# Kernel optimization log

Measured on AMD Instinct MI355X. Metric: run time of the kernel, lower is better.

## Reference

```python
import math
import jax, jax.numpy as jnp
import numpy as np

N_HEADS = 8
WINDOW = 4


def _get_relative_embeddings(emb, length, window):
    # emb: [1, 2*window+1, k_channels] -> [1, 2*length-1, k_channels]
    pad_length = max(length - (window + 1), 0)
    start = max(window + 1 - length, 0)
    if pad_length > 0:
        emb = jnp.pad(emb, ((0, 0), (pad_length, pad_length), (0, 0)))
    return emb[:, start:start + 2 * length - 1]


def _relative_position_to_absolute_position(x):
    # x: [b, h, l, 2l-1] -> [b, h, l, l] (skewing trick)
    b, h, l, _ = x.shape
    x = jnp.pad(x, ((0, 0), (0, 0), (0, 0), (0, 1)))
    x_flat = x.reshape(b, h, l * 2 * l)
    x_flat = jnp.pad(x_flat, ((0, 0), (0, 0), (0, l - 1)))
    return x_flat.reshape(b, h, l + 1, 2 * l - 1)[:, :, :l, l - 1:]


def _absolute_position_to_relative_position(x):
    # x: [b, h, l, l] -> [b, h, l, 2l-1]
    b, h, l, _ = x.shape
    x = jnp.pad(x, ((0, 0), (0, 0), (0, 0), (0, l - 1)))
    x_flat = x.reshape(b, h, l * l + l * (l - 1))
    x_flat = jnp.pad(x_flat, ((0, 0), (0, 0), (l, 0)))
    return x_flat.reshape(b, h, l, 2 * l)[:, :, :, 1:]


def setup_inputs() -> dict:
    key = jax.random.key(0)
    ks = jax.random.split(key, 12)
    b, t, d = 4, 1024, 512
    kc = d // N_HEADS
    s = 1.0 / math.sqrt(d)
    return {
        "x": jax.random.normal(ks[0], (b, t, d), jnp.float32),
        "c": jax.random.normal(ks[1], (b, t, d), jnp.float32),
        "wq": jax.random.normal(ks[2], (d, d), jnp.float32) * s,
        "bq": jnp.zeros((d,), jnp.float32),
        "wk": jax.random.normal(ks[3], (d, d), jnp.float32) * s,
        "bk": jnp.zeros((d,), jnp.float32),
        "wv": jax.random.normal(ks[4], (d, d), jnp.float32) * s,
        "bv": jnp.zeros((d,), jnp.float32),
        "wo": jax.random.normal(ks[5], (d, d), jnp.float32) * s,
        "bo": jnp.zeros((d,), jnp.float32),
        "emb_rel_k": jax.random.normal(ks[6], (1, 2 * WINDOW + 1, kc), jnp.float32) * kc ** -0.5,
        "emb_rel_v": jax.random.normal(ks[7], (1, 2 * WINDOW + 1, kc), jnp.float32) * kc ** -0.5,
    }


def reference(x, c, wq, bq, wk, bk, wv, bv, wo, bo, emb_rel_k, emb_rel_v):
    b, t, d = x.shape
    h = N_HEADS
    kc = d // h
    inv_sqrt = 1.0 / math.sqrt(kc)

    # 1x1 conv projections (pointwise matmul)
    q = x @ wq + bq   # [b, t, d]
    k = c @ wk + bk
    v = c @ wv + bv

    # Faithful reshape as in source: [b, t, d] -> [b, h, kc, t] -> [b, h, t, kc]
    q = q.reshape(b, h, kc, t).transpose(0, 1, 3, 2)
    k = k.reshape(b, h, kc, t).transpose(0, 1, 3, 2)
    v = v.reshape(b, h, kc, t).transpose(0, 1, 3, 2)

    scores = jnp.einsum('bhtd,bhsd->bhts', q, k) * inv_sqrt  # [b,h,t,t]

    # relative key logits
    key_rel = _get_relative_embeddings(emb_rel_k, t, WINDOW)[0]  # [2t-1, kc]
    rel_logits = jnp.einsum('bhtd,md->bhtm', q, key_rel)          # [b,h,t,2t-1]
    scores_local = _relative_position_to_absolute_position(rel_logits) * inv_sqrt
    scores = scores + scores_local

    p_attn = jax.nn.softmax(scores, axis=-1)
    output = jnp.einsum('bhts,bhsd->bhtd', p_attn, v)  # [b,h,t,kc]

    # relative value contribution
    rel_weights = _absolute_position_to_relative_position(p_attn)  # [b,h,t,2t-1]
    val_rel = _get_relative_embeddings(emb_rel_v, t, WINDOW)[0]    # [2t-1, kc]
    output = output + jnp.einsum('bhtm,md->bhtd', rel_weights, val_rel)

    # Faithful output reshape: [b,h,t,kc] -> [b,h,kc,t] -> [b,t,d]
    output = output.transpose(0, 1, 3, 2).reshape(b, t, d)
    out = output @ wo + bo
    return out
```

## Files before the change

### kernel.cpp

```cpp
#include <hip/hip_runtime.h>
#include <hip/hip_bf16.h>

#define NB 4
#define NT 1024
#define ND 512
#define NH 8
#define NKC 64

typedef __bf16 bf16x8 __attribute__((ext_vector_type(8)));
typedef float f32x4 __attribute__((ext_vector_type(4)));
typedef unsigned int u32;

__device__ __forceinline__ f32x4 MFMA(bf16x8 a, bf16x8 b, f32x4 c) {
    return __builtin_amdgcn_mfma_f32_16x16x32_bf16(a, b, c, 0, 0, 0);
}
__device__ __forceinline__ unsigned short f2bu(float v) {
    __hip_bfloat16 b = __float2bfloat16(v);
    return *(unsigned short*)&b;
}
__device__ __forceinline__ void split1(float v, unsigned short& h, unsigned short& l)
{
    __hip_bfloat16 hb = __float2bfloat16(v);
    float r = v - __bfloat162float(hb);
    __hip_bfloat16 lb = __float2bfloat16(r);
    h = *(unsigned short*)&hb;
    l = *(unsigned short*)&lb;
}
__device__ __forceinline__ void splitpack(const float4 a, const float4 b, uint4& h, uint4& l)
{
    union { unsigned short u[8]; uint4 v; } H, L;
    const float f[8] = {a.x, a.y, a.z, a.w, b.x, b.y, b.z, b.w};
    #pragma unroll
    for (int j = 0; j < 8; ++j) split1(f[j], H.u[j], L.u[j]);
    h = H.v; l = L.v;
}
__device__ __forceinline__ void gl16(const unsigned short* g, unsigned short* l) {
    __builtin_amdgcn_global_load_lds(
        (const __attribute__((address_space(1))) u32*)g,
        (__attribute__((address_space(3))) u32*)l, 16, 0, 0);
}

__global__ __launch_bounds__(256)
void splitT_kernel(const float* __restrict__ w0, const float* __restrict__ w1,
                   const float* __restrict__ w2, const float* __restrict__ w3,
                   unsigned short* __restrict__ wT)
{
    __shared__ float tl[32][33];
    const float* w = (blockIdx.z == 0) ? w0 : (blockIdx.z == 1) ? w1
                   : (blockIdx.z == 2) ? w2 : w3;
    unsigned short* hi = wT + (size_t)blockIdx.z * 2 * (ND * ND);
    unsigned short* lo = hi + ND * ND;
    const int t = threadIdx.x;
    const int x0 = blockIdx.x * 32, y0 = blockIdx.y * 32;
    {
        const int r = t >> 3, c = (t & 7) * 4;
        const float4 v = *(const float4*)&w[(size_t)(y0 + r) * ND + x0 + c];
        tl[r][c] = v.x; tl[r][c+1] = v.y; tl[r][c+2] = v.z; tl[r][c+3] = v.w;
    }
    __syncthreads();
    {
        const int nr = t >> 3, k4 = (t & 7) * 4;
        unsigned short hh[4], ll[4];
        #pragma unroll
        for (int j = 0; j < 4; ++j) split1(tl[k4 + j][nr], hh[j], ll[j]);
        ushort4 h = make_ushort4(hh[0], hh[1], hh[2], hh[3]);
        ushort4 l = make_ushort4(ll[0], ll[1], ll[2], ll[3]);
        *(ushort4*)&hi[(size_t)(x0 + nr) * ND + y0 + k4] = h;
        *(ushort4*)&lo[(size_t)(x0 + nr) * ND + y0 + k4] = l;
    }
}

__global__ __launch_bounds__(256, 3)
void proj_mfma(const float* __restrict__ x, const float* __restrict__ cc,
               const unsigned short* __restrict__ wT,
               const float* __restrict__ bq, const float* __restrict__ bk,
               const float* __restrict__ bv,
               unsigned short* __restrict__ qh_o, unsigned short* __restrict__ ql_o,
               unsigned short* __restrict__ kh_o, unsigned short* __restrict__ vh_o)
{
    __shared__ unsigned short smem[13312];
    unsigned short* Ah = smem;
    unsigned short* Al = smem + 2560;
    unsigned short* Bh = smem + 5120;
    unsigned short* Bl = smem + 9216;
    unsigned short* Tr = smem;

    const int hw = blockIdx.x + 4 * blockIdx.y + 256 * blockIdx.z;
    const int swz = (hw & 7) * 96 + (hw >> 3);
    const int xt = swz & 3;
    const int yt = (swz >> 2) & 63;
    const int which = swz >> 8;

    const float* A_g = (which == 0) ? x : cc;
    const unsigned short* Bh_g = wT + (size_t)which * 2 * (ND * ND);
    const unsigned short* Bl_g = Bh_g + ND * ND;
    const float* bias = (which == 0) ? bq : (which == 1) ? bk : bv;

    const int tid = threadIdx.x, l = tid & 63, w = tid >> 6;
    const int quad = l >> 4, lc = l & 15;
    const int wm = w & 1, wn = w >> 1;
    const int n0 = xt * 128, m0 = yt * 64;

    const int am = tid >> 2, ak = (tid & 3) * 8;
    const size_t aG = (size_t)(m0 + am) * ND + ak;

    const int lr = l >> 2, lc4 = l & 3;
    const int lcs = lc4 ^ ((lr >> 1) & 3);
    const unsigned short* bsrcH0 = Bh_g + (size_t)(n0 + w * 32 + lr) * ND + lcs * 8;
    const unsigned short* bsrcH1 = bsrcH0 + 16 * ND;
    const unsigned short* bsrcL0 = Bl_g + (size_t)(n0 + w * 32 + lr) * ND + lcs * 8;
    const unsigned short* bsrcL1 = bsrcL0 + 16 * ND;
    unsigned short* bdstH0 = Bh + (w * 32) * 32;
    unsigned short* bdstH1 = Bh + (w * 32 + 16) * 32;
    unsigned short* bdstL0 = Bl + (w * 32) * 32;
    unsigned short* bdstL1 = Bl + (w * 32 + 16) * 32;

    float4 ra0 = *(const float4*)&A_g[aG];
    float4 ra1 = *(const float4*)&A_g[aG + 4];
    uint4 h0, l0;
    splitpack(ra0, ra1, h0, l0);

    const int fsw = (lc >> 1) & 3;
    const int bchunk = (quad ^ fsw) * 8;

    f32x4 acc[2][4];
    #pragma unroll
    for (int mi = 0; mi < 2; ++mi)
        #pragma unroll
        for (int ni = 0; ni < 4; ++ni) acc[mi][ni] = (f32x4){0.f, 0.f, 0.f, 0.f};

    for (int k0 = 0; k0 < ND; k0 += 32) {
        __syncthreads();
        {
            *(uint4*)&Ah[am * 40 + ak] = h0;
            *(uint4*)&Al[am * 40 + ak] = l0;
            gl16(bsrcH0 + k0, bdstH0);
            gl16(bsrcH1 + k0, bdstH1);
            gl16(bsrcL0 + k0, bdstL0);
            gl16(bsrcL1 + k0, bdstL1);
        }
        __syncthreads();
        if (k0 + 32 < ND) {
            const size_t aN = aG + k0 + 32;
            ra0 = *(const float4*)&A_g[aN];
            ra1 = *(const float4*)&A_g[aN + 4];
        }

        bf16x8 ah[2], al2[2], bh[4], bl[4];
        #pragma unroll
        for (int mi = 0; mi < 2; ++mi) {
            const int ar = (wm * 32 + mi * 16 + lc) * 40 + quad * 8;
            ah[mi] = *(const bf16x8*)&Ah[ar];
            al2[mi] = *(const bf16x8*)&Al[ar];
        }
        #pragma unroll
        for (int ni = 0; ni < 4; ++ni) {
            const int br = (wn * 64 + ni * 16 + lc) * 32 + bchunk;
            bh[ni] = *(const bf16x8*)&Bh[br];
            bl[ni] = *(const bf16x8*)&Bl[br];
        }
        #pragma unroll
        for (int mi = 0; mi < 2; ++mi)
            #pragma unroll
            for (int ni = 0; ni < 4; ++ni) {
                acc[mi][ni] = MFMA(al2[mi], bh[ni], acc[mi][ni]);
                acc[mi][ni] = MFMA(ah[mi], bl[ni], acc[mi][ni]);
                acc[mi][ni] = MFMA(ah[mi], bh[ni], acc[mi][ni]);
            }
        if (k0 + 32 < ND) splitpack(ra0, ra1, h0, l0);
    }

    const int bb = m0 >> 10, tt0 = m0 & 1023;
    const int hh = tt0 >> 7, cch0 = (tt0 & 127) >> 1;
    const int bh_idx = bb * NH + hh;

    if (which == 2) {
        #pragma unroll
        for (int ni = 0; ni < 4; ++ni) {
            const int n = n0 + wn * 64 + ni * 16 + lc;
            const float bval = bias[n];
            #pragma unroll
            for (int mi = 0; mi < 2; ++mi)
                #pragma unroll
                for (int r = 0; r < 4; ++r) {
                    const int mloc = wm * 32 + mi * 16 + quad * 4 + r;
                    const int cch = cch0 + (mloc >> 1);
                    const int t = (mloc & 1) * 512 + n;
                    vh_o[(((size_t)bh_idx * 16 + (t >> 6)) * 64 + cch) * 64 + (t & 63)] =
                        f2bu(acc[mi][ni][r] + bval);
                }
        }
        return;
    }

    const int npass = (which == 0) ? 2 : 1;
    unsigned short* outp[2] = {(which == 0) ? qh_o : kh_o, ql_o};

    for (int pass = 0; pass < npass; ++pass) {
        __syncthreads();
        #pragma unroll
        for (int ni = 0; ni < 4; ++ni) {
            const int nloc = wn * 64 + ni * 16 + lc;
            const float bval = bias[n0 + nloc];
            #pragma unroll
            for (int mi = 0; mi < 2; ++mi)
                #pragma unroll
                for (int r = 0; r < 4; ++r) {
                    const int mloc = wm * 32 + mi * 16 + quad * 4 + r;
                    const float val = acc[mi][ni][r] + bval;
                    unsigned short hs, ls;
                    if (which == 0) { split1(val, hs, ls); }
                    else { hs = f2bu(val); ls = 0; }
                    Tr[((mloc & 1) * 128 + nloc) * 40 + (mloc >> 1)] =
                        (pass == 0) ? hs : ls;
                }
        }
        __syncthreads();
        {
            const int t = (tid >> 7) * 512 + n0 + (tid & 127);
            const size_t oa = ((size_t)bh_idx * NT + t) * NKC + cch0;
            const uint4 v0 = *(const uint4*)&Tr[tid * 40];
            const uint4 v1 = *(const uint4*)&Tr[tid * 40 + 8];
            const uint4 v2 = *(const uint4*)&Tr[tid * 40 + 16];
            const uint4 v3 = *(const uint4*)&Tr[tid * 40 + 24];
            *(uint4*)&outp[pass][oa]      = v0;
            *(uint4*)&outp[pass][oa + 8]  = v1;
            *(uint4*)&outp[pass][oa + 16] = v2;
            *(uint4*)&outp[pass][oa + 24] = v3;
        }
    }
}

__global__ __launch_bounds__(256, 4)
void outproj_mfma(const unsigned short* __restrict__ a_g,
                  const unsigned short* __restrict__ wTh,
                  const float* __restrict__ bo, float* __restrict__ out)
{
    __shared__ unsigned short smem2[6144];
    unsigned short* As = smem2;
    unsigned short* Bh = smem2 + 2048;
    unsigned short* Bl = smem2 + 4096;
    const unsigned short* Bl_g = wTh + ND * ND;
    const int tid = threadIdx.x, l = tid & 63, w = tid >> 6;
    const int quad = l >> 4, lc = l & 15;
    const int wm = w & 1, wn = w >> 1;

    const int hw = blockIdx.x + 8 * blockIdx.y;
    const int swz = (hw & 7) * 64 + (hw >> 3);
    const int n0 = (swz & 7) * 64, m0 = (swz >> 3) * 64;

    const int lr = l >> 2, lc4 = l & 3;
    const int lcs = lc4 ^ ((lr >> 1) & 3);
    const unsigned short* asrc  = a_g + (size_t)(m0 + w * 16 + lr) * ND + lcs * 8;
    const unsigned short* bhsrc = wTh + (size_t)(n0 + w * 16 + lr) * ND + lcs * 8;
    const unsigned short* blsrc = Bl_g + (size_t)(n0 + w * 16 + lr) * ND + lcs * 8;
    unsigned short* adst = As + (w * 16) * 32;
    unsigned short* bhdst = Bh + (w * 16) * 32;
    unsigned short* bldst = Bl + (w * 16) * 32;

    const int fsw = (lc >> 1) & 3;
    const int chunk = (quad ^ fsw) * 8;

    f32x4 acc[2][2];
    #pragma unroll
    for (int mi = 0; mi < 2; ++mi)
        #pragma unroll
        for (int ni = 0; ni < 2; ++ni) acc[mi][ni] = (f32x4){0.f, 0.f, 0.f, 0.f};

    for (int k0 = 0; k0 < ND; k0 += 32) {
        __syncthreads();
        gl16(asrc + k0, adst);
        gl16(bhsrc + k0, bhdst);
        gl16(blsrc + k0, bldst);
        __syncthreads();

        bf16x8 ab[2], bhf[2], blf[2];
        #pragma unroll
        for (int mi = 0; mi < 2; ++mi)
            ab[mi] = *(const bf16x8*)&As[(wm * 32 + mi * 16 + lc) * 32 + chunk];
        #pragma unroll
        for (int ni = 0; ni < 2; ++ni) {
            const int br = (wn * 32 + ni * 16 + lc) * 32 + chunk;
            bhf[ni] = *(const bf16x8*)&Bh[br];
            blf[ni] = *(const bf16x8*)&Bl[br];
        }
        #pragma unroll
        for (int mi = 0; mi < 2; ++mi)
            #pragma unroll
            for (int ni = 0; ni < 2; ++ni) {
                acc[mi][ni] = MFMA(ab[mi], bhf[ni], acc[mi][ni]);
                acc[mi][ni] = MFMA(ab[mi], blf[ni], acc[mi][ni]);
            }
    }

    #pragma unroll
    for (int ni = 0; ni < 2; ++ni) {
        const int n = n0 + wn * 32 + ni * 16 + lc;
        const float bval = bo[n];
        #pragma unroll
        for (int mi = 0; mi < 2; ++mi)
            #pragma unroll
            for (int r = 0; r < 4; ++r) {
                const int m = m0 + wm * 32 + mi * 16 + quad * 4 + r;
                out[(size_t)m * ND + n] = acc[mi][ni][r] + bval;
            }
    }
}

__global__ __launch_bounds__(512, 4)
void attn_mfma(const unsigned short* __restrict__ qh_g, const unsigned short* __restrict__ ql_g,
               const unsigned short* __restrict__ kh_g,
               const unsigned short* __restrict__ vh_g,
               const float* __restrict__ embk, const float* __restrict__ embv,
               unsigned short* __restrict__ ath)
{
    __shared__ unsigned short smem[33792];
    unsigned short* Ev  = smem + 16384;
    unsigned short* Ps  = smem + 18944;
    float* bandv = (float*)(smem + 32256);
    unsigned short* EkH = smem + 18944;
    unsigned short* EkL = EkH + 1152;

    const int tid = threadIdx.x, l = tid & 63, w = tid >> 6;
    const int quad = l >> 4, lc = l & 15;
    const int g = w & 3;
    const int h = w >> 2;

    const int hw = blockIdx.x + 16 * blockIdx.y + 128 * blockIdx.z;
    const int swz = (hw & 7) * 64 + (hw >> 3);
    const int q0 = (swz & 15) * 64;
    const int hh = (swz >> 4) & 7, bb = swz >> 7;

    const int sBeg = h * 512;
    const int bh = bb * NH + hh;
    const size_t qkBase = (size_t)bh * NT * NKC;
    const size_t vtBase = (size_t)bh * (16 * 64 * 64);

    unsigned short* Ksh = smem + h * 4096;
    unsigned short* Vsh = smem + 8192 + h * 4096;

    const int tl = tid & 255;
    const int rr = tl >> 3, cc8 = tl & 7;
    const int cs = cc8 ^ (rr & 7);
    const unsigned short* kSrc = kh_g + qkBase + (size_t)(sBeg + rr) * NKC + cs * 8;
    const unsigned short* vSrc = vh_g + vtBase + (size_t)(sBeg >> 6) * 4096 + rr * 64 + cs * 8;
    const int wvh = tl >> 6;
    unsigned short* dK = Ksh + wvh * 512;
    unsigned short* dV = Vsh + wvh * 512;

    for (int idx = tid; idx < 16 * 72; idx += 512) {
        const int d = idx / 72, kc = idx - d * 72;
        const float v = (d < 9 && kc < 64) ? embk[d * 64 + kc] : 0.f;
        unsigned short hs, ls;
        split1(v, hs, ls);
        EkH[idx] = hs;
        EkL[idx] = ls;
    }
    for (int idx = tid; idx < 64 * 40; idx += 512) {
        const int c = idx / 40, d = idx - c * 40;
        Ev[idx] = f2bu((d < 9) ? embv[d * 64 + c] : 0.f);
    }
    __syncthreads();

    bf16x8 qh[2], ql[2];
    {
        const int qg = q0 + g * 16 + lc;
        const size_t qa = qkBase + (size_t)qg * NKC + quad * 8;
        qh[0] = *(const bf16x8*)&qh_g[qa];
        qh[1] = *(const bf16x8*)&qh_g[qa + 32];
        ql[0] = *(const bf16x8*)&ql_g[qa];
        ql[1] = *(const bf16x8*)&ql_g[qa + 32];
    }

    {
        f32x4 accB = (f32x4){0.f, 0.f, 0.f, 0.f};
        #pragma unroll
        for (int kk = 0; kk < 2; ++kk) {
            const bf16x8 ebh = *(const bf16x8*)&EkH[lc * 72 + kk * 32 + quad * 8];
            const bf16x8 ebl = *(const bf16x8*)&EkL[lc * 72 + kk * 32 + quad * 8];
            accB = MFMA(ql[kk], ebh, accB);
            accB = MFMA(qh[kk], ebl, accB);
            accB = MFMA(qh[kk], ebh, accB);
        }
        __syncthreads();
        if (h == 0 && lc <= 8) {
            #pragma unroll
            for (int r = 0; r < 4; ++r)
                bandv[(g * 16 + quad * 4 + r) * 12 + lc] = accB[r];
        }
    }
    unsigned short* P = Ps + w * 1664;
    {
        const int zr = l >> 2, zc = 64 + (l & 3) * 8;
        *(uint4*)&P[zr * 104 + zc] = (uint4){0u, 0u, 0u, 0u};
    }

    const int swz8 = lc & 7;

    f32x4 O[4];
    #pragma unroll
    for (int ci = 0; ci < 4; ++ci) O[ci] = (f32x4){0.f, 0.f, 0.f, 0.f};
    float l_run[4] = {0.f, 0.f, 0.f, 0.f};
    bool prevdiag = false;

    for (int s0 = sBeg; s0 < sBeg + 512; s0 += 64) {
        __syncthreads();
        gl16(kSrc, dK);  gl16(kSrc + 2048, dK + 2048);
        gl16(vSrc, dV);  gl16(vSrc + 2048, dV + 2048);
        kSrc += 4096; vSrc += 4096;
        __syncthreads();

        const int sd = s0 - q0;
        const bool diag = (sd >= -64) && (sd <= 64);

        f32x4 S[4];
        #pragma unroll
        for (int ni = 0; ni < 4; ++ni) {
            f32x4 a = (f32x4){0.f, 0.f, 0.f, 0.f};
            #pragma unroll
            for (int kk = 0; kk < 2; ++kk) {
                const bf16x8 kb = *(const bf16x8*)
                    &Ksh[(ni * 16 + lc) * 64 + ((kk * 4 + quad) ^ swz8) * 8];
                a = MFMA(ql[kk], kb, a);
                a = MFMA(qh[kk], kb, a);
            }
            S[ni] = a;
        }

        if (diag) {
            #pragma unroll
            for (int ni = 0; ni < 4; ++ni)
                #pragma unroll
                for (int r = 0; r < 4; ++r) {
                    const int ql64 = g * 16 + quad * 4 + r;
                    const int dp4 = (s0 + ni * 16 + lc) - (q0 + ql64) + 4;
                    if (dp4 >= 0 && dp4 <= 8) S[ni][r] += bandv[ql64 * 12 + dp4];
                }
        }
        #pragma unroll
        for (int ni = 0; ni < 4; ++ni)
            #pragma unroll
            for (int r = 0; r < 4; ++r)
                S[ni][r] = __expf(S[ni][r] * 0.125f);
        #pragma unroll
        for (int r = 0; r < 4; ++r)
            l_run[r] += S[0][r] + S[1][r] + S[2][r] + S[3][r];

        if (diag || prevdiag) {
            const int zr = l >> 2, zc = 64 + (l & 3) * 4;
            *(ushort4*)&P[zr * 104 + zc] = make_ushort4(0, 0, 0, 0);
        }
        if (diag) {
            #pragma unroll
            for (int ni = 0; ni < 4; ++ni)
                #pragma unroll
                for (int r = 0; r < 4; ++r) {
                    const int prow = quad * 4 + r;
                    const unsigned short pb = f2bu(S[ni][r]);
                    P[prow * 104 + ni * 16 + lc] = pb;
                    const int dp4 = (s0 + ni * 16 + lc) - (q0 + g * 16 + prow) + 4;
                    if (dp4 >= 0 && dp4 <= 8) P[prow * 104 + 64 + dp4] = pb;
                }
        } else {
            #pragma unroll
            for (int ni = 0; ni < 4; ++ni)
                #pragma unroll
                for (int r = 0; r < 4; ++r) {
                    const int prow = quad * 4 + r;
                    P[prow * 104 + ni * 16 + lc] = f2bu(S[ni][r]);
                }
        }

        #pragma unroll
        for (int ks = 0; ks < 2; ++ks) {
            const bf16x8 pa = *(const bf16x8*)&P[lc * 104 + ks * 32 + quad * 8];
            #pragma unroll
            for (int ci = 0; ci < 4; ++ci) {
                const bf16x8 vb = *(const bf16x8*)
                    &Vsh[(ci * 16 + lc) * 64 + ((ks * 4 + quad) ^ swz8) * 8];
                O[ci] = MFMA(pa, vb, O[ci]);
            }
        }
        {
            const bf16x8 pa = *(const bf16x8*)&P[lc * 104 + 64 + quad * 8];
            #pragma unroll
            for (int ci = 0; ci < 4; ++ci) {
                const bf16x8 vb = *(const bf16x8*)&Ev[(ci * 16 + lc) * 40 + quad * 8];
                O[ci] = MFMA(pa, vb, O[ci]);
            }
        }
        prevdiag = diag;
    }

    #pragma unroll
    for (int r = 0; r < 4; ++r) {
        float v = l_run[r];
        v += __shfl_xor(v, 1); v += __shfl_xor(v, 2);
        v += __shfl_xor(v, 4); v += __shfl_xor(v, 8);
        l_run[r] = v;
    }

    __syncthreads();
    float* Oex = (float*)smem;
    float* l1s = bandv;
    const int qloc0 = g * 16 + quad * 4;

    if (h == 1) {
        #pragma unroll
        for (int ci = 0; ci < 4; ++ci)
            #pragma unroll
            for (int r = 0; r < 4; ++r)
                Oex[(qloc0 + r) * 64 + ci * 16 + lc] = O[ci][r];
        if (lc == 0) {
            #pragma unroll
            for (int r = 0; r < 4; ++r)
                l1s[qloc0 + r] = l_run[r];
        }
    }
    __syncthreads();
    if (h == 0) {
        float linv[4];
        #pragma unroll
        for (int r = 0; r < 4; ++r)
            linv[r] = 1.f / (l_run[r] + l1s[qloc0 + r]);
        #pragma unroll
        for (int ci = 0; ci < 4; ++ci) {
            const int c = ci * 16 + lc;
            const int row = hh * 128 + 2 * c + (q0 >> 9);
            unsigned short o[4];
            #pragma unroll
            for (int r = 0; r < 4; ++r)
                o[r] = f2bu((O[ci][r] + Oex[(qloc0 + r) * 64 + c]) * linv[r]);
            *(ushort4*)&ath[((size_t)bb * NT + row) * ND + (q0 & 511) + qloc0] =
                make_ushort4(o[0], o[1], o[2], o[3]);
        }
    }
}

extern "C" void kernel_launch(void* const* d_in, const int* in_sizes, int n_in,
                              void* d_out, int out_size, void* d_ws, size_t ws_size,
                              hipStream_t stream) {
    const float* x    = (const float*)d_in[0];
    const float* c    = (const float*)d_in[1];
    const float* wq   = (const float*)d_in[2];
    const float* bq   = (const float*)d_in[3];
    const float* wk   = (const float*)d_in[4];
    const float* bk   = (const float*)d_in[5];
    const float* wv   = (const float*)d_in[6];
    const float* bv   = (const float*)d_in[7];
    const float* wo   = (const float*)d_in[8];
    const float* bo   = (const float*)d_in[9];
    const float* embk = (const float*)d_in[10];
    const float* embv = (const float*)d_in[11];

    unsigned short* u16 = (unsigned short*)d_ws;
    const size_t M = 1024 * 1024;
    unsigned short* wT  = u16;
    unsigned short* qh  = u16 + 2 * M;
    unsigned short* ql  = u16 + 4 * M;
    unsigned short* kh  = u16 + 6 * M;
    unsigned short* vh  = u16 + 8 * M;
    unsigned short* ath = u16 + 10 * M;

    splitT_kernel<<<dim3(16, 16, 4), 256, 0, stream>>>(wq, wk, wv, wo, wT);

    proj_mfma<<<dim3(4, 64, 3), 256, 0, stream>>>(x, c, wT, bq, bk, bv,
                                                  qh, ql, kh, vh);

    attn_mfma<<<dim3(16, 8, 4), 512, 0, stream>>>(qh, ql, kh, vh,
                                                  embk, embv, ath);

    outproj_mfma<<<dim3(8, 64), 256, 0, stream>>>(ath,
                                                  wT + (size_t)3 * 2 * ND * ND,
                                                  bo, (float*)d_out);
}
```

Before: 149.6 us.

## Load K/V MFMA fragments directly from global memory, dropping LDS staging

Replaces the shared-memory staging of K and V tiles, which needed two block-wide barriers per iteration, with per-lane direct global loads of the bf16x8 MFMA fragments. The shared-memory footprint roughly halves, which may allow more blocks per CU. The cost is that each group of waves sharing a head half now fetches the same K/V rows separately, multiplying global/L2 traffic. The loads may also be less coalesced and their latency is exposed without explicit staging.

```diff
diff --git a/kernel.cpp b/kernel.cpp
--- a/kernel.cpp
+++ b/kernel.cpp
@@ -314,11 +314,11 @@
                const float* __restrict__ embk, const float* __restrict__ embv,
                unsigned short* __restrict__ ath)
 {
-    __shared__ unsigned short smem[33792];
-    unsigned short* Ev  = smem + 16384;
-    unsigned short* Ps  = smem + 18944;
-    float* bandv = (float*)(smem + 32256);
-    unsigned short* EkH = smem + 18944;
+    __shared__ unsigned short smem[17408];
+    unsigned short* Ps  = smem;
+    unsigned short* Ev  = smem + 13312;
+    float* bandv = (float*)(smem + 15872);
+    unsigned short* EkH = smem;
     unsigned short* EkL = EkH + 1152;
 
     const int tid = threadIdx.x, l = tid & 63, w = tid >> 6;
@@ -335,18 +335,6 @@
     const int bh = bb * NH + hh;
     const size_t qkBase = (size_t)bh * NT * NKC;
     const size_t vtBase = (size_t)bh * (16 * 64 * 64);
-
-    unsigned short* Ksh = smem + h * 4096;
-    unsigned short* Vsh = smem + 8192 + h * 4096;
-
-    const int tl = tid & 255;
-    const int rr = tl >> 3, cc8 = tl & 7;
-    const int cs = cc8 ^ (rr & 7);
-    const unsigned short* kSrc = kh_g + qkBase + (size_t)(sBeg + rr) * NKC + cs * 8;
-    const unsigned short* vSrc = vh_g + vtBase + (size_t)(sBeg >> 6) * 4096 + rr * 64 + cs * 8;
-    const int wvh = tl >> 6;
-    unsigned short* dK = Ksh + wvh * 512;
-    unsigned short* dV = Vsh + wvh * 512;
 
     for (int idx = tid; idx < 16 * 72; idx += 512) {
         const int d = idx / 72, kc = idx - d * 72;
@@ -394,8 +382,10 @@
         const int zr = l >> 2, zc = 64 + (l & 3) * 8;
         *(uint4*)&P[zr * 104 + zc] = (uint4){0u, 0u, 0u, 0u};
     }
-
-    const int swz8 = lc & 7;
+    __syncthreads();
+
+    const unsigned short* kF = kh_g + qkBase + (size_t)(sBeg + lc) * NKC + quad * 8;
+    const unsigned short* vF = vh_g + vtBase + (size_t)(sBeg >> 6) * 4096 + lc * 64 + quad * 8;
 
     f32x4 O[4];
     #pragma unroll
@@ -404,28 +394,29 @@
     bool prevdiag = false;
 
     for (int s0 = sBeg; s0 < sBeg + 512; s0 += 64) {
-        __syncthreads();
-        gl16(kSrc, dK);  gl16(kSrc + 2048, dK + 2048);
-        gl16(vSrc, dV);  gl16(vSrc + 2048, dV + 2048);
-        kSrc += 4096; vSrc += 4096;
-        __syncthreads();
-
+        const int st = s0 - sBeg;
         const int sd = s0 - q0;
         const bool diag = (sd >= -64) && (sd <= 64);
 
         f32x4 S[4];
         #pragma unroll
         for (int ni = 0; ni < 4; ++ni) {
+            const bf16x8 k0 = *(const bf16x8*)&kF[(size_t)(st + ni * 16) * NKC];
+            const bf16x8 k1 = *(const bf16x8*)&kF[(size_t)(st + ni * 16) * NKC + 32];
             f32x4 a = (f32x4){0.f, 0.f, 0.f, 0.f};
-            #pragma unroll
-            for (int kk = 0; kk < 2; ++kk) {
-                const bf16x8 kb = *(const bf16x8*)
-                    &Ksh[(ni * 16 + lc) * 64 + ((kk * 4 + quad) ^ swz8) * 8];
-                a = MFMA(ql[kk], kb, a);
-                a = MFMA(qh[kk], kb, a);
-            }
+            a = MFMA(ql[0], k0, a);
+            a = MFMA(qh[0], k0, a);
+            a = MFMA(ql[1], k1, a);
+            a = MFMA(qh[1], k1, a);
             S[ni] = a;
         }
+
+        bf16x8 vf[4][2];
+        #pragma unroll
+        for (int ci = 0; ci < 4; ++ci)
+            #pragma unroll
+            for (int ks = 0; ks < 2; ++ks)
+                vf[ci][ks] = *(const bf16x8*)&vF[(size_t)(st >> 6) * 4096 + ci * 1024 + ks * 32];
 
         if (diag) {
             #pragma unroll
@@ -475,11 +466,8 @@
         for (int ks = 0; ks < 2; ++ks) {
             const bf16x8 pa = *(const bf16x8*)&P[lc * 104 + ks * 32 + quad * 8];
             #pragma unroll
-            for (int ci = 0; ci < 4; ++ci) {
-                const bf16x8 vb = *(const bf16x8*)
-                    &Vsh[(ci * 16 + lc) * 64 + ((ks * 4 + quad) ^ swz8) * 8];
-                O[ci] = MFMA(pa, vb, O[ci]);
-            }
+            for (int ci = 0; ci < 4; ++ci)
+                O[ci] = MFMA(pa, vf[ci][ks], O[ci]);
         }
         {
             const bf16x8 pa = *(const bf16x8*)&P[lc * 104 + 64 + quad * 8];
```

After: 184.4 us. 1.23x slower.

## Double-buffer LDS in projection GEMMs and skip relative-value MFMA off-diagonal

Applied to the files above, without the earlier changes.

The input and output projection GEMMs now use two LDS buffers. The next K-slice is staged while the current one is computed, which leaves one barrier per step instead of two and lets global loads overlap MFMA work. The attention kernel now runs the band relative-value MFMA, and zeroes its P columns, only on diagonal tiles rather than on every tile. Doubling shared memory may lower occupancy for the projection kernels, which request 3 and 4 blocks per CU.

```diff
diff --git a/kernel.cpp b/kernel.cpp
--- a/kernel.cpp
+++ b/kernel.cpp
@@ -78,11 +78,7 @@
                unsigned short* __restrict__ qh_o, unsigned short* __restrict__ ql_o,
                unsigned short* __restrict__ kh_o, unsigned short* __restrict__ vh_o)
 {
-    __shared__ unsigned short smem[13312];
-    unsigned short* Ah = smem;
-    unsigned short* Al = smem + 2560;
-    unsigned short* Bh = smem + 5120;
-    unsigned short* Bl = smem + 9216;
+    __shared__ unsigned short smem[26624];
     unsigned short* Tr = smem;
 
     const int hw = blockIdx.x + 4 * blockIdx.y + 256 * blockIdx.z;
@@ -110,64 +106,81 @@
     const unsigned short* bsrcH1 = bsrcH0 + 16 * ND;
     const unsigned short* bsrcL0 = Bl_g + (size_t)(n0 + w * 32 + lr) * ND + lcs * 8;
     const unsigned short* bsrcL1 = bsrcL0 + 16 * ND;
-    unsigned short* bdstH0 = Bh + (w * 32) * 32;
-    unsigned short* bdstH1 = Bh + (w * 32 + 16) * 32;
-    unsigned short* bdstL0 = Bl + (w * 32) * 32;
-    unsigned short* bdstL1 = Bl + (w * 32 + 16) * 32;
+
+    const int fsw = (lc >> 1) & 3;
+    const int bchunk = (quad ^ fsw) * 8;
+
+    f32x4 acc[2][4];
+    #pragma unroll
+    for (int mi = 0; mi < 2; ++mi)
+        #pragma unroll
+        for (int ni = 0; ni < 4; ++ni) acc[mi][ni] = (f32x4){0.f, 0.f, 0.f, 0.f};
+
+    auto STAGE = [&](unsigned short* base, int k0, const uint4& h, const uint4& lo4) {
+        *(uint4*)&base[am * 40 + ak] = h;
+        *(uint4*)&base[2560 + am * 40 + ak] = lo4;
+        gl16(bsrcH0 + k0, base + 5120 + w * 1024);
+        gl16(bsrcH1 + k0, base + 5120 + w * 1024 + 512);
+        gl16(bsrcL0 + k0, base + 9216 + w * 1024);
+        gl16(bsrcL1 + k0, base + 9216 + w * 1024 + 512);
+    };
+    auto COMPUTE = [&](const unsigned short* base) {
+        bf16x8 ah[2], al2[2], bhf[4], blf[4];
+        #pragma unroll
+        for (int mi = 0; mi < 2; ++mi) {
+            const int ar = (wm * 32 + mi * 16 + lc) * 40 + quad * 8;
+            ah[mi]  = *(const bf16x8*)&base[ar];
+            al2[mi] = *(const bf16x8*)&base[2560 + ar];
+        }
+        #pragma unroll
+        for (int ni = 0; ni < 4; ++ni) {
+            const int br = (wn * 64 + ni * 16 + lc) * 32 + bchunk;
+            bhf[ni] = *(const bf16x8*)&base[5120 + br];
+            blf[ni] = *(const bf16x8*)&base[9216 + br];
+        }
+        #pragma unroll
+        for (int mi = 0; mi < 2; ++mi)
+            #pragma unroll
+            for (int ni = 0; ni < 4; ++ni) {
+                acc[mi][ni] = MFMA(al2[mi], bhf[ni], acc[mi][ni]);
+                acc[mi][ni] = MFMA(ah[mi], blf[ni], acc[mi][ni]);
+                acc[mi][ni] = MFMA(ah[mi], bhf[ni], acc[mi][ni]);
+            }
+    };
 
     float4 ra0 = *(const float4*)&A_g[aG];
     float4 ra1 = *(const float4*)&A_g[aG + 4];
     uint4 h0, l0;
     splitpack(ra0, ra1, h0, l0);
-
-    const int fsw = (lc >> 1) & 3;
-    const int bchunk = (quad ^ fsw) * 8;
-
-    f32x4 acc[2][4];
-    #pragma unroll
-    for (int mi = 0; mi < 2; ++mi)
-        #pragma unroll
-        for (int ni = 0; ni < 4; ++ni) acc[mi][ni] = (f32x4){0.f, 0.f, 0.f, 0.f};
-
-    for (int k0 = 0; k0 < ND; k0 += 32) {
-        __syncthreads();
+    STAGE(smem, 0, h0, l0);
+    ra0 = *(const float4*)&A_g[aG + 32];
+    ra1 = *(const float4*)&A_g[aG + 36];
+    __syncthreads();
+
+    #pragma unroll
+    for (int k0 = 0; k0 < ND; k0 += 64) {
         {
-            *(uint4*)&Ah[am * 40 + ak] = h0;
-            *(uint4*)&Al[am * 40 + ak] = l0;
-            gl16(bsrcH0 + k0, bdstH0);
-            gl16(bsrcH1 + k0, bdstH1);
-            gl16(bsrcL0 + k0, bdstL0);
-            gl16(bsrcL1 + k0, bdstL1);
-        }
-        __syncthreads();
-        if (k0 + 32 < ND) {
-            const size_t aN = aG + k0 + 32;
-            ra0 = *(const float4*)&A_g[aN];
-            ra1 = *(const float4*)&A_g[aN + 4];
-        }
-
-        bf16x8 ah[2], al2[2], bh[4], bl[4];
-        #pragma unroll
-        for (int mi = 0; mi < 2; ++mi) {
-            const int ar = (wm * 32 + mi * 16 + lc) * 40 + quad * 8;
-            ah[mi] = *(const bf16x8*)&Ah[ar];
-            al2[mi] = *(const bf16x8*)&Al[ar];
-        }
-        #pragma unroll
-        for (int ni = 0; ni < 4; ++ni) {
-            const int br = (wn * 64 + ni * 16 + lc) * 32 + bchunk;
-            bh[ni] = *(const bf16x8*)&Bh[br];
-            bl[ni] = *(const bf16x8*)&Bl[br];
-        }
-        #pragma unroll
-        for (int mi = 0; mi < 2; ++mi)
-            #pragma unroll
-            for (int ni = 0; ni < 4; ++ni) {
-                acc[mi][ni] = MFMA(al2[mi], bh[ni], acc[mi][ni]);
-                acc[mi][ni] = MFMA(ah[mi], bl[ni], acc[mi][ni]);
-                acc[mi][ni] = MFMA(ah[mi], bh[ni], acc[mi][ni]);
-            }
-        if (k0 + 32 < ND) splitpack(ra0, ra1, h0, l0);
+            splitpack(ra0, ra1, h0, l0);
+            STAGE(smem + 13312, k0 + 32, h0, l0);
+            if (k0 + 64 < ND) {
+                ra0 = *(const float4*)&A_g[aG + k0 + 64];
+                ra1 = *(const float4*)&A_g[aG + k0 + 68];
+            }
+            COMPUTE(smem);
+            __syncthreads();
+        }
+        {
+            if (k0 + 64 < ND) {
+                splitpack(ra0, ra1, h0, l0);
+                STAGE(smem, k0 + 64, h0, l0);
+                if (k0 + 96 < ND) {
+                    ra0 = *(const float4*)&A_g[aG + k0 + 96];
+                    ra1 = *(const float4*)&A_g[aG + k0 + 100];
+                }
+            }
+            COMPUTE(smem + 13312);
+            __syncthreads();
+        }
     }
 
     const int bb = m0 >> 10, tt0 = m0 & 1023;
@@ -236,10 +249,7 @@
                   const unsigned short* __restrict__ wTh,
                   const float* __restrict__ bo, float* __restrict__ out)
 {
-    __shared__ unsigned short smem2[6144];
-    unsigned short* As = smem2;
-    unsigned short* Bh = smem2 + 2048;
-    unsigned short* Bl = smem2 + 4096;
+    __shared__ unsigned short smem2[12288];
     const unsigned short* Bl_g = wTh + ND * ND;
     const int tid = threadIdx.x, l = tid & 63, w = tid >> 6;
     const int quad = l >> 4, lc = l & 15;
@@ -254,9 +264,6 @@
     const unsigned short* asrc  = a_g + (size_t)(m0 + w * 16 + lr) * ND + lcs * 8;
     const unsigned short* bhsrc = wTh + (size_t)(n0 + w * 16 + lr) * ND + lcs * 8;
     const unsigned short* blsrc = Bl_g + (size_t)(n0 + w * 16 + lr) * ND + lcs * 8;
-    unsigned short* adst = As + (w * 16) * 32;
-    unsigned short* bhdst = Bh + (w * 16) * 32;
-    unsigned short* bldst = Bl + (w * 16) * 32;
 
     const int fsw = (lc >> 1) & 3;
     const int chunk = (quad ^ fsw) * 8;
@@ -267,22 +274,21 @@
         #pragma unroll
         for (int ni = 0; ni < 2; ++ni) acc[mi][ni] = (f32x4){0.f, 0.f, 0.f, 0.f};
 
-    for (int k0 = 0; k0 < ND; k0 += 32) {
-        __syncthreads();
-        gl16(asrc + k0, adst);
-        gl16(bhsrc + k0, bhdst);
-        gl16(blsrc + k0, bldst);
-        __syncthreads();
-
+    auto STAGE = [&](unsigned short* base, int k0) {
+        gl16(asrc + k0, base + w * 512);
+        gl16(bhsrc + k0, base + 2048 + w * 512);
+        gl16(blsrc + k0, base + 4096 + w * 512);
+    };
+    auto COMPUTE = [&](const unsigned short* base) {
         bf16x8 ab[2], bhf[2], blf[2];
         #pragma unroll
         for (int mi = 0; mi < 2; ++mi)
-            ab[mi] = *(const bf16x8*)&As[(wm * 32 + mi * 16 + lc) * 32 + chunk];
+            ab[mi] = *(const bf16x8*)&base[(wm * 32 + mi * 16 + lc) * 32 + chunk];
         #pragma unroll
         for (int ni = 0; ni < 2; ++ni) {
             const int br = (wn * 32 + ni * 16 + lc) * 32 + chunk;
-            bhf[ni] = *(const bf16x8*)&Bh[br];
-            blf[ni] = *(const bf16x8*)&Bl[br];
+            bhf[ni] = *(const bf16x8*)&base[2048 + br];
+            blf[ni] = *(const bf16x8*)&base[4096 + br];
         }
         #pragma unroll
         for (int mi = 0; mi < 2; ++mi)
@@ -291,6 +297,18 @@
                 acc[mi][ni] = MFMA(ab[mi], bhf[ni], acc[mi][ni]);
                 acc[mi][ni] = MFMA(ab[mi], blf[ni], acc[mi][ni]);
             }
+    };
+
+    STAGE(smem2, 0);
+    __syncthreads();
+    #pragma unroll
+    for (int k0 = 0; k0 < ND; k0 += 64) {
+        STAGE(smem2 + 6144, k0 + 32);
+        COMPUTE(smem2);
+        __syncthreads();
+        if (k0 + 64 < ND) STAGE(smem2, k0 + 64);
+        COMPUTE(smem2 + 6144);
+        __syncthreads();
     }
 
     #pragma unroll
@@ -401,7 +419,6 @@
     #pragma unroll
     for (int ci = 0; ci < 4; ++ci) O[ci] = (f32x4){0.f, 0.f, 0.f, 0.f};
     float l_run[4] = {0.f, 0.f, 0.f, 0.f};
-    bool prevdiag = false;
 
     for (int s0 = sBeg; s0 < sBeg + 512; s0 += 64) {
         __syncthreads();
@@ -446,11 +463,11 @@
         for (int r = 0; r < 4; ++r)
             l_run[r] += S[0][r] + S[1][r] + S[2][r] + S[3][r];
 
-        if (diag || prevdiag) {
-            const int zr = l >> 2, zc = 64 + (l & 3) * 4;
-            *(ushort4*)&P[zr * 104 + zc] = make_ushort4(0, 0, 0, 0);
-        }
         if (diag) {
+            {
+                const int zr = l >> 2, zc = 64 + (l & 3) * 4;
+                *(ushort4*)&P[zr * 104 + zc] = make_ushort4(0, 0, 0, 0);
+            }
             #pragma unroll
             for (int ni = 0; ni < 4; ++ni)
                 #pragma unroll
@@ -481,7 +498,7 @@
                 O[ci] = MFMA(pa, vb, O[ci]);
             }
         }
-        {
+        if (diag) {
             const bf16x8 pa = *(const bf16x8*)&P[lc * 104 + 64 + quad * 8];
             #pragma unroll
             for (int ci = 0; ci < 4; ++ci) {
@@ -489,7 +506,6 @@
                 O[ci] = MFMA(pa, vb, O[ci]);
             }
         }
-        prevdiag = diag;
     }
 
     #pragma unroll
```

Measured after the change: 149.5 us, median of 2. Within noise of the previous version (-0.1%).
